# Kernel optimization log

Measured on AMD Instinct MI355X. Metric: run time of the kernel, lower is better.

## Reference

```python
import jax, jax.numpy as jnp
import numpy as np

D = 4          # latent_dims = 2 * 2
POS = 3        # pos_dims = 2 + pos_sorted
HID = 20       # encoder hidden width
LOG_2PI = float(np.log(2.0 * np.pi))


def _fill_scale_tril(vec, d):
    # FillScaleTriL(diag=Exp): lower-tri fill, exp on the diagonal
    idx = jnp.tril_indices(d)
    L = jnp.zeros((d, d), vec.dtype).at[idx].set(vec)
    dg = jnp.diag(L)
    return L - jnp.diag(dg) + jnp.diag(jnp.exp(dg))


def _forward(x, eps, enc_w1, enc_b1, enc_wx, enc_bx, enc_wl, enc_bl,
             dec_w, dec_b, A, b_kf, q_param):
    d = A.shape[0]
    I = jnp.eye(d, dtype=x.dtype)
    # ---- encoder (shared params over time axis, per-object) ----
    h = jax.nn.relu(x @ enc_w1 + enc_b1)            # [T+1, N, HID]
    xhat = h @ enc_wx + enc_bx                       # [T+1, N, d]
    sigma = jnp.exp(0.5 * (h @ enc_wl + enc_bl))     # [T+1, N, d]
    R = sigma[..., :, None] * I                      # diag obs covs [T+1, N, d, d]
    m0, P0 = xhat[0], R[0]                           # initial state per object [N, d]
    zm, zC = xhat[1:], R[1:]                         # measurements [T, N, d], [T, N, d, d]
    # ---- Q = L L^T via CholeskyOuterProduct(FillScaleTriL(q_param)) ----
    L = _fill_scale_tril(q_param, d)
    Q = L @ L.T
    logN = jnp.log(jnp.asarray(zm.shape[1], x.dtype))

    def filter_one(m0_, P0_):
        # PDA Kalman filter for one track over all N measurements per step
        def step(carry, inp):
            m, P = carry
            z, Rz = inp                              # [N, d], [N, d, d]
            mp = A @ m + b_kf
            Pp = A @ P @ A.T + Q
            S = Pp[None] + Rz                        # innovation covs [N, d, d]
            innov = z - mp                           # [N, d]
            sol = jnp.linalg.solve(S, innov[..., None])[..., 0]
            _, logdet = jnp.linalg.slogdet(S)
            ll = -0.5 * (jnp.einsum('nd,nd->n', innov, sol) + logdet + d * LOG_2PI)
            w = jax.nn.softmax(ll)                   # association weights
            # K = Pp S^{-1} (S, Pp symmetric)
            K = jnp.linalg.solve(S, jnp.broadcast_to(Pp, S.shape)).transpose(0, 2, 1)
            mi = mp + jnp.einsum('nij,nj->ni', K, innov)
            Pi = (I - K) @ Pp
            mu = jnp.einsum('n,ni->i', w, mi)
            diff = mi - mu
            Pu = jnp.einsum('n,nij->ij', w, Pi + diff[:, :, None] * diff[:, None, :])
            Pu = 0.5 * (Pu + Pu.T)
            step_ll = jax.nn.logsumexp(ll) - logN    # marginal over associations
            return (mu, Pu), (mu, Pu, mp, Pp, step_ll)

        _, (fm, fP, pm, pP, lls) = jax.lax.scan(step, (m0_, P0_), (zm, zC))

        # ---- RTS smoother (backward pass) ----
        def back(carry, inp):
            ms, Ps = carry
            mf, Pf = inp
            mp = A @ mf + b_kf
            Pp = A @ Pf @ A.T + Q
            G = jnp.linalg.solve(Pp, A @ Pf).T       # Pf A^T Pp^{-1}
            ms2 = mf + G @ (ms - mp)
            Ps2 = Pf + G @ (Ps - Pp) @ G.T
            Ps2 = 0.5 * (Ps2 + Ps2.T)
            return (ms2, Ps2), (ms2, Ps2)

        _, (sm, sP) = jax.lax.scan(back, (fm[-1], fP[-1]), (fm[:-1], fP[:-1]), reverse=True)
        sm = jnp.concatenate([sm, fm[-1:]], 0)
        sP = jnp.concatenate([sP, fP[-1:]], 0)
        return fm, fP, pm, pP, sm, sP, lls

    # vmap over tracks; out_axes=1 puts object axis second ([T, N, ...])
    fm, fP, pm, pP, sm, sP, lls = jax.vmap(filter_one, in_axes=0, out_axes=1)(m0, P0)

    # reparameterized sample from q (smoothed posterior) and decode
    Lc = jnp.linalg.cholesky(sP + 1e-5 * I)          # [T, N, d, d]
    z_recon = sm + jnp.einsum('tnij,tnj->tni', Lc, eps)
    x_recon = z_recon @ dec_w + dec_b                # [T, N, POS]
    return x_recon


def setup_inputs() -> dict:
    key = jax.random.key(0)
    ks = jax.random.split(key, 12)
    Tp1, N = 2049, 64
    s = lambda fan: 1.0 / np.sqrt(fan)
    return {
        'x': jax.random.normal(ks[0], (Tp1, N, POS), jnp.float32),
        'eps': jax.random.normal(ks[1], (Tp1 - 1, N, D), jnp.float32),
        'enc_w1': jax.random.normal(ks[2], (POS, HID), jnp.float32) * s(POS),
        'enc_b1': jnp.zeros((HID,), jnp.float32),
        'enc_wx': jax.random.normal(ks[3], (HID, D), jnp.float32) * s(HID),
        'enc_bx': jnp.zeros((D,), jnp.float32),
        'enc_wl': jax.random.normal(ks[4], (HID, D), jnp.float32) * s(HID),
        'enc_bl': jnp.zeros((D,), jnp.float32),
        'dec_w': jax.random.normal(ks[5], (D, POS), jnp.float32) * s(D),
        'dec_b': jnp.zeros((POS,), jnp.float32),
        'A': jnp.eye(D, dtype=jnp.float32) + 0.01 * jax.random.normal(ks[6], (D, D), jnp.float32),
        'b_kf': jnp.zeros((D,), jnp.float32),
        'q_param': 0.02 * jax.random.normal(ks[7], (D * (D + 1) // 2,), jnp.float32),
    }


def reference(x, eps, enc_w1, enc_b1, enc_wx, enc_bx, enc_wl, enc_bl,
              dec_w, dec_b, A, b_kf, q_param):
    return _forward(x, eps, enc_w1, enc_b1, enc_wx, enc_bx, enc_wl, enc_bl,
                    dec_w, dec_b, A, b_kf, q_param)
```

## Files before the change

### kernel.cpp

```cpp
#include <hip/hip_runtime.h>
#include <math.h>

#define D4   4
#define NB   64
#define T    2048
#define TP1  2049
#define HID  20
#define POS  3
#define CH   64
#define CLEN 32

#define OFF_XHAT  0
#define OFF_SIGMA (TP1*NB*4)
#define OFF_FR    (2*TP1*NB*4)
#define OFF_C     (OFF_FR + T*NB*16)
#define OFF_E     (OFF_C + NB*CH*36)

template<int CTRL, int RM>
__device__ __forceinline__ float dpp_sum_step(float v) {
  int t = __builtin_amdgcn_update_dpp(0, __float_as_int(v), CTRL, RM, 0xF, true);
  return v + __int_as_float(t);
}
__device__ __forceinline__ float wsum_v(float v) {
  v = dpp_sum_step<0x111, 0xF>(v);
  v = dpp_sum_step<0x112, 0xF>(v);
  v = dpp_sum_step<0x114, 0xF>(v);
  v = dpp_sum_step<0x118, 0xF>(v);
  v = dpp_sum_step<0x142, 0xA>(v);
  v = dpp_sum_step<0x143, 0xC>(v);
  return v;
}
__device__ __forceinline__ float rdlane(float v, int l) {
  return __int_as_float(__builtin_amdgcn_readlane(__float_as_int(v), l));
}

__device__ __forceinline__ float inv4(const float a[4][4], float inv[4][4]) {
  float s0 = a[0][0]*a[1][1] - a[1][0]*a[0][1];
  float s1 = a[0][0]*a[1][2] - a[1][0]*a[0][2];
  float s2 = a[0][0]*a[1][3] - a[1][0]*a[0][3];
  float s3 = a[0][1]*a[1][2] - a[1][1]*a[0][2];
  float s4 = a[0][1]*a[1][3] - a[1][1]*a[0][3];
  float s5 = a[0][2]*a[1][3] - a[1][2]*a[0][3];
  float c5 = a[2][2]*a[3][3] - a[3][2]*a[2][3];
  float c4 = a[2][1]*a[3][3] - a[3][1]*a[2][3];
  float c3 = a[2][1]*a[3][2] - a[3][1]*a[2][2];
  float c2 = a[2][0]*a[3][3] - a[3][0]*a[2][3];
  float c1 = a[2][0]*a[3][2] - a[3][0]*a[2][2];
  float c0 = a[2][0]*a[3][1] - a[3][0]*a[2][1];
  float det = s0*c5 - s1*c4 + s2*c3 + s3*c2 - s4*c1 + s5*c0;
  float id = __fdividef(1.0f, det);
  inv[0][0] = ( a[1][1]*c5 - a[1][2]*c4 + a[1][3]*c3) * id;
  inv[0][1] = (-a[0][1]*c5 + a[0][2]*c4 - a[0][3]*c3) * id;
  inv[0][2] = ( a[3][1]*s5 - a[3][2]*s4 + a[3][3]*s3) * id;
  inv[0][3] = (-a[2][1]*s5 + a[2][2]*s4 - a[2][3]*s3) * id;
  inv[1][0] = (-a[1][0]*c5 + a[1][2]*c2 - a[1][3]*c1) * id;
  inv[1][1] = ( a[0][0]*c5 - a[0][2]*c2 + a[0][3]*c1) * id;
  inv[1][2] = (-a[3][0]*s5 + a[3][2]*s2 - a[3][3]*s1) * id;
  inv[1][3] = ( a[2][0]*s5 - a[2][2]*s2 + a[2][3]*s1) * id;
  inv[2][0] = ( a[1][0]*c4 - a[1][1]*c2 + a[1][3]*c0) * id;
  inv[2][1] = (-a[0][0]*c4 + a[0][1]*c2 - a[0][3]*c0) * id;
  inv[2][2] = ( a[3][0]*s4 - a[3][1]*s2 + a[3][3]*s0) * id;
  inv[2][3] = (-a[2][0]*s4 + a[2][1]*s2 - a[2][3]*s0) * id;
  inv[3][0] = (-a[1][0]*c3 + a[1][1]*c1 - a[1][2]*c0) * id;
  inv[3][1] = ( a[0][0]*c3 - a[0][1]*c1 + a[0][2]*c0) * id;
  inv[3][2] = (-a[3][0]*s3 + a[3][1]*s1 - a[3][2]*s0) * id;
  inv[3][3] = ( a[2][0]*s3 - a[2][1]*s1 + a[2][2]*s0) * id;
  return det;
}

__device__ __forceinline__ void build_Q(const float* __restrict__ qp, float Q[4][4]) {
  float L[4][4] = {{0.f,0.f,0.f,0.f},{0.f,0.f,0.f,0.f},{0.f,0.f,0.f,0.f},{0.f,0.f,0.f,0.f}};
  L[0][0] = expf(qp[0]);
  L[1][0] = qp[1]; L[1][1] = expf(qp[2]);
  L[2][0] = qp[3]; L[2][1] = qp[4]; L[2][2] = expf(qp[5]);
  L[3][0] = qp[6]; L[3][1] = qp[7]; L[3][2] = qp[8]; L[3][3] = expf(qp[9]);
#pragma unroll
  for (int r = 0; r < 4; ++r)
#pragma unroll
    for (int c = 0; c < 4; ++c) {
      float v = 0.f;
#pragma unroll
      for (int k = 0; k < 4; ++k) v += L[r][k] * L[c][k];
      Q[r][c] = v;
    }
}

__device__ __forceinline__ void load_A_b_Q(const float* __restrict__ Ag,
                                           const float* __restrict__ bg,
                                           const float* __restrict__ qp,
                                           float A[4][4], float b[4], float Q[4][4]) {
#pragma unroll
  for (int r = 0; r < 4; ++r) {
    b[r] = bg[r];
#pragma unroll
    for (int c = 0; c < 4; ++c) A[r][c] = Ag[r * 4 + c];
  }
  build_Q(qp, Q);
}

__device__ __forceinline__ void load_state_raw(const float* __restrict__ p,
                                               float mf[4], float Pf[4][4]) {
  float4 r0 = *(const float4*)&p[0];
  float4 r1 = *(const float4*)&p[4];
  float4 r2 = *(const float4*)&p[8];
  float4 r3 = *(const float4*)&p[12];
  float rW = __fdividef(1.0f, r0.x);
  mf[0]=r0.y*rW; mf[1]=r0.z*rW; mf[2]=r0.w*rW; mf[3]=r1.x*rW;
  Pf[0][0]=fmaf(r1.y,rW,-mf[0]*mf[0]);
  Pf[0][1]=fmaf(r1.z,rW,-mf[0]*mf[1]); Pf[1][0]=Pf[0][1];
  Pf[0][2]=fmaf(r1.w,rW,-mf[0]*mf[2]); Pf[2][0]=Pf[0][2];
  Pf[0][3]=fmaf(r2.x,rW,-mf[0]*mf[3]); Pf[3][0]=Pf[0][3];
  Pf[1][1]=fmaf(r2.y,rW,-mf[1]*mf[1]);
  Pf[1][2]=fmaf(r2.z,rW,-mf[1]*mf[2]); Pf[2][1]=Pf[1][2];
  Pf[1][3]=fmaf(r2.w,rW,-mf[1]*mf[3]); Pf[3][1]=Pf[1][3];
  Pf[2][2]=fmaf(r3.x,rW,-mf[2]*mf[2]);
  Pf[2][3]=fmaf(r3.y,rW,-mf[2]*mf[3]); Pf[3][2]=Pf[2][3];
  Pf[3][3]=fmaf(r3.z,rW,-mf[3]*mf[3]);
}

__global__ void k_encoder(const float* __restrict__ x,
                          const float* __restrict__ w1, const float* __restrict__ b1,
                          const float* __restrict__ wx, const float* __restrict__ bx,
                          const float* __restrict__ wl, const float* __restrict__ bl,
                          float* __restrict__ xhat, float* __restrict__ sigma) {
  int idx = blockIdx.x * blockDim.x + threadIdx.x;
  if (idx >= TP1 * NB) return;
  float x0 = x[idx*3+0], x1 = x[idx*3+1], x2 = x[idx*3+2];
  float xh[4], lm[4];
#pragma unroll
  for (int k = 0; k < 4; ++k) { xh[k] = bx[k]; lm[k] = bl[k]; }
#pragma unroll
  for (int j = 0; j < HID; ++j) {
    float h = x0*w1[0*HID+j] + x1*w1[1*HID+j] + x2*w1[2*HID+j] + b1[j];
    h = fmaxf(h, 0.0f);
#pragma unroll
    for (int k = 0; k < 4; ++k) { xh[k] += h * wx[j*4+k]; lm[k] += h * wl[j*4+k]; }
  }
  *(float4*)&xhat[(size_t)idx*4]  = make_float4(xh[0], xh[1], xh[2], xh[3]);
  *(float4*)&sigma[(size_t)idx*4] = make_float4(expf(0.5f*lm[0]), expf(0.5f*lm[1]),
                                                expf(0.5f*lm[2]), expf(0.5f*lm[3]));
}

__global__ void __launch_bounds__(256, 1) k_filter(
    const float* __restrict__ xhat, const float* __restrict__ sigma,
    const float* __restrict__ Ag, const float* __restrict__ bg,
    const float* __restrict__ qp,
    float* __restrict__ fr) {
  const int fi  = blockIdx.x;
  const int tid = threadIdx.x;
  const int wv  = tid >> 6;
  const int n   = tid & 63;

  __shared__ __align__(16) float xch[2][16];

  int r, c;
  if (n < 10) {
    r = (n < 4) ? 0 : (n < 7) ? 1 : (n < 9) ? 2 : 3;
    c = (n < 4) ? n : (n < 7) ? n - 3 : (n < 9) ? n - 5 : 3;
  } else if (n < 14) { r = n - 10; c = 0; }
  else { r = 0; c = 0; }

  float ar0 = Ag[r*4+0], ar1 = Ag[r*4+1], ar2 = Ag[r*4+2], ar3 = Ag[r*4+3];
  float ac0 = Ag[c*4+0], ac1 = Ag[c*4+1], ac2 = Ag[c*4+2], ac3 = Ag[c*4+3];
  float qmask = (n < 10) ? 1.0f : 0.0f;
  float pmask = (n >= 10 && n < 14) ? 1.0f : 0.0f;
  float wp0 = (ar0*ac0) * qmask;
  float wp1 = (ar0*ac1 + ar1*ac0) * qmask;
  float wp2 = (ar0*ac2 + ar2*ac0) * qmask;
  float wp3 = (ar0*ac3 + ar3*ac0) * qmask;
  float wp4 = (ar1*ac1) * qmask;
  float wp5 = (ar1*ac2 + ar2*ac1) * qmask;
  float wp6 = (ar1*ac3 + ar3*ac1) * qmask;
  float wp7 = (ar2*ac2) * qmask;
  float wp8 = (ar2*ac3 + ar3*ac2) * qmask;
  float wp9 = (ar3*ac3) * qmask;

  float initv;
  {
    int trir = r*(r+1)/2, tric = c*(c+1)/2;
    float Lr[4], Lc[4];
#pragma unroll
    for (int k = 0; k < 4; ++k) {
      Lr[k] = (k > r) ? 0.0f : (k == r ? expf(qp[trir+r]) : qp[trir+k]);
      Lc[k] = (k > c) ? 0.0f : (k == c ? expf(qp[tric+c]) : qp[tric+k]);
    }
    float Qe = Lr[0]*Lc[0] + Lr[1]*Lc[1] + Lr[2]*Lc[2] + Lr[3]*Lc[3];
    if (n < 10)      initv = Qe;
    else if (n < 14) initv = bg[n-10];
    else             initv = 0.0f;
  }

  float4 A0, A1, A2, A3;
  {
    float4 m0 = *(const float4*)&xhat[fi*4];
    float4 s0 = *(const float4*)&sigma[fi*4];
    A0 = make_float4(1.0f, m0.x, m0.y, m0.z);
    A1 = make_float4(m0.w,
                     fmaf(m0.x, m0.x, s0.x), m0.x*m0.y, m0.x*m0.z);
    A2 = make_float4(m0.x*m0.w,
                     fmaf(m0.y, m0.y, s0.y), m0.y*m0.z, m0.y*m0.w);
    A3 = make_float4(fmaf(m0.z, m0.z, s0.z), m0.z*m0.w,
                     fmaf(m0.w, m0.w, s0.w), 0.0f);
  }

  float4 zz  = *(const float4*)&xhat[(size_t)(NB + n)*4];
  float4 sgc = *(const float4*)&sigma[(size_t)(NB + n)*4];

#pragma unroll 2
  for (int t = 0; t < T; ++t) {
    int nr = (t + 2 <= TP1 - 1) ? (t + 2) : (TP1 - 1);
    float4 zn  = *(const float4*)&xhat[((size_t)nr*NB + n)*4];
    float4 sgn = *(const float4*)&sigma[((size_t)nr*NB + n)*4];

    float rW = __fdividef(1.0f, A0.x);
    float dotq =
        ((fmaf(wp0, A1.y, wp1*A1.z) + fmaf(wp2, A1.w, wp3*A2.x)) +
         (fmaf(wp4, A2.y, wp5*A2.z) + fmaf(wp6, A2.w, wp7*A3.x))) +
        fmaf(wp8, A3.y, wp9*A3.z);
    float wdr = fmaf(ar0, A0.y, ar1*A0.z) + fmaf(ar2, A0.w, ar3*A1.x);
    float wdc = fmaf(ac0, A0.y, ac1*A0.z) + fmaf(ac2, A0.w, ac3*A1.x);
    float Amur = wdr * rW, Amuc = wdc * rW;
    float pe = fmaf(dotq, rW, initv);
    pe = fmaf(pmask, Amur, pe);
    pe = fmaf(-qmask, Amur*Amuc, pe);

    float p00 = rdlane(pe, 0), p01 = rdlane(pe, 1), p02 = rdlane(pe, 2), p03 = rdlane(pe, 3);
    float p11 = rdlane(pe, 4), p12 = rdlane(pe, 5), p13 = rdlane(pe, 6);
    float p22 = rdlane(pe, 7), p23 = rdlane(pe, 8), p33 = rdlane(pe, 9);
    float mp0 = rdlane(pe,10), mp1 = rdlane(pe,11), mp2 = rdlane(pe,12), mp3 = rdlane(pe,13);

    float s00 = p00 + sgc.x, s11 = p11 + sgc.y, s22 = p22 + sgc.z, s33 = p33 + sgc.w;
    float s01 = p01, s02 = p02, s03 = p03, s12 = p12, s13 = p13, s23 = p23;

    float m0_ = s00*s11 - s01*s01;
    float m1_ = s00*s12 - s01*s02;
    float m2_ = s00*s13 - s01*s03;
    float m3_ = s01*s12 - s11*s02;
    float m4_ = s01*s13 - s11*s03;
    float m5_ = s02*s13 - s12*s03;
    float n5_ = s22*s33 - s23*s23;
    float n4_ = s12*s33 - s13*s23;
    float n3_ = s12*s23 - s13*s22;
    float n2_ = s02*s33 - s03*s23;
    float n1_ = s02*s23 - s03*s22;
    float det = (fmaf(m0_, n5_, -(m1_*n4_)) + fmaf(m2_, n3_, m3_*n2_)) +
                fmaf(m5_, m5_, -(m4_*n1_));
    float id  = __fdividef(1.0f, det);
    float rsd = __builtin_amdgcn_rsqf(det);
    float a00_ = ( s11*n5_ - s12*n4_ + s13*n3_);
    float a01_ = (-s01*n5_ + s02*n4_ - s03*n3_);
    float a02_ = ( s13*m5_ - s23*m4_ + s33*m3_);
    float a03_ = (-s12*m5_ + s22*m4_ - s23*m3_);
    float a11_ = ( s00*n5_ - s02*n2_ + s03*n1_);
    float a12_ = (-s03*m5_ + s23*m2_ - s33*m1_);
    float a13_ = ( s02*m5_ - s22*m2_ + s23*m1_);
    float a22_ = ( s03*m4_ - s13*m2_ + s33*m0_);
    float a23_ = (-s02*m4_ + s12*m2_ - s23*m0_);
    float a33_ = ( s02*m3_ - s12*m1_ + s22*m0_);

    float iv0 = zz.x - mp0, iv1 = zz.y - mp1, iv2 = zz.z - mp2, iv3 = zz.w - mp3;
    float ya0 = fmaf(a00_, iv0, a01_*iv1) + fmaf(a02_, iv2, a03_*iv3);
    float ya1 = fmaf(a01_, iv0, a11_*iv1) + fmaf(a12_, iv2, a13_*iv3);
    float ya2 = fmaf(a02_, iv0, a12_*iv1) + fmaf(a22_, iv2, a23_*iv3);
    float ya3 = fmaf(a03_, iv0, a13_*iv1) + fmaf(a23_, iv2, a33_*iv3);
    float quad = (fmaf(iv0, ya0, iv1*ya1) + fmaf(iv2, ya2, iv3*ya3)) * id;

    float wi = __expf(-0.5f * quad) * rsd;

    float y0 = ya0*id, y1 = ya1*id, y2 = ya2*id, y3 = ya3*id;
    float mi0 = fmaf(-sgc.x, y0, zz.x);
    float mi1 = fmaf(-sgc.y, y1, zz.y);
    float mi2 = fmaf(-sgc.z, y2, zz.z);
    float mi3 = fmaf(-sgc.w, y3, zz.w);

    const int par = t & 1;
    float* lb = xch[par];

    if (wv == 0) {
      float cW  = wsum_v(wi);
      float cm0 = wsum_v(wi*mi0);
      float cm1 = wsum_v(wi*mi1);
      float cm2 = wsum_v(wi*mi2);
      float cm3 = wsum_v(wi*mi3);
      if (n == 63) {
        *(float4*)&lb[0] = make_float4(cW, cm0, cm1, cm2);
        lb[4] = cm3;
      }
    } else if (wv == 1) {
      float t0 = sgc.x * id;
      float X00 = fmaf(mi0, mi0, sgc.x) - (t0*sgc.x)*a00_;
      float X01 = fmaf(mi0, mi1, -(t0*sgc.y)*a01_);
      float X02 = fmaf(mi0, mi2, -(t0*sgc.z)*a02_);
      float X03 = fmaf(mi0, mi3, -(t0*sgc.w)*a03_);
      float c00 = wsum_v(wi*X00);
      float c01 = wsum_v(wi*X01);
      float c02 = wsum_v(wi*X02);
      float c03 = wsum_v(wi*X03);
      if (n == 63) { lb[5]=c00; lb[6]=c01; lb[7]=c02; lb[8]=c03; }
    } else if (wv == 2) {
      float t1 = sgc.y * id;
      float X11 = fmaf(mi1, mi1, sgc.y) - (t1*sgc.y)*a11_;
      float X12 = fmaf(mi1, mi2, -(t1*sgc.z)*a12_);
      float X13 = fmaf(mi1, mi3, -(t1*sgc.w)*a13_);
      float c11 = wsum_v(wi*X11);
      float c12 = wsum_v(wi*X12);
      float c13 = wsum_v(wi*X13);
      if (n == 63) { lb[9]=c11; lb[10]=c12; lb[11]=c13; }
    } else {
      float t2 = sgc.z * id;
      float t3 = sgc.w * id;
      float X22 = fmaf(mi2, mi2, sgc.z) - (t2*sgc.z)*a22_;
      float X23 = fmaf(mi2, mi3, -(t2*sgc.w)*a23_);
      float X33 = fmaf(mi3, mi3, sgc.w) - (t3*sgc.w)*a33_;
      float c22 = wsum_v(wi*X22);
      float c23 = wsum_v(wi*X23);
      float c33 = wsum_v(wi*X33);
      if (n == 63) {
        *(float2*)&lb[12] = make_float2(c22, c23);
        lb[14] = c33;
      }
    }

    __syncthreads();

    A0 = *(const float4*)&xch[par][0];
    A1 = *(const float4*)&xch[par][4];
    A2 = *(const float4*)&xch[par][8];
    A3 = *(const float4*)&xch[par][12];

    if (wv == 0 && n == 0) {
      float* fp = &fr[((size_t)t*NB + fi)*16];
      *(float4*)&fp[0]  = A0;
      *(float4*)&fp[4]  = A1;
      *(float4*)&fp[8]  = A2;
      *(float4*)&fp[12] = A3;
    }
    zz = zn; sgc = sgn;
  }
}

struct Map { float G[4][4]; float c[4]; float Dm[4][4]; };

__device__ __forceinline__ void map_identity(Map& M) {
#pragma unroll
  for (int r = 0; r < 4; ++r) {
    M.c[r] = 0.f;
#pragma unroll
    for (int cc = 0; cc < 4; ++cc) { M.G[r][cc] = (r==cc)?1.f:0.f; M.Dm[r][cc] = 0.f; }
  }
}

__device__ __forceinline__ void compose(const Map& F, const Map& Sm, Map& R) {
  float G[4][4], cv[4], V[4][4], Dn[4][4];
#pragma unroll
  for (int r = 0; r < 4; ++r)
#pragma unroll
    for (int c = 0; c < 4; ++c)
      G[r][c] = F.G[r][0]*Sm.G[0][c] + F.G[r][1]*Sm.G[1][c]
              + F.G[r][2]*Sm.G[2][c] + F.G[r][3]*Sm.G[3][c];
#pragma unroll
  for (int r = 0; r < 4; ++r)
    cv[r] = F.c[r] + F.G[r][0]*Sm.c[0] + F.G[r][1]*Sm.c[1]
                   + F.G[r][2]*Sm.c[2] + F.G[r][3]*Sm.c[3];
#pragma unroll
  for (int r = 0; r < 4; ++r)
#pragma unroll
    for (int c = 0; c < 4; ++c)
      V[r][c] = F.G[r][0]*Sm.Dm[0][c] + F.G[r][1]*Sm.Dm[1][c]
              + F.G[r][2]*Sm.Dm[2][c] + F.G[r][3]*Sm.Dm[3][c];
#pragma unroll
  for (int r = 0; r < 4; ++r)
#pragma unroll
    for (int c = r; c < 4; ++c) {
      float v = F.Dm[r][c] + V[r][0]*F.G[c][0] + V[r][1]*F.G[c][1]
                           + V[r][2]*F.G[c][2] + V[r][3]*F.G[c][3];
      Dn[r][c] = v; Dn[c][r] = v;
    }
#pragma unroll
  for (int r = 0; r < 4; ++r) {
    R.c[r] = cv[r];
#pragma unroll
    for (int c = 0; c < 4; ++c) { R.G[r][c] = G[r][c]; R.Dm[r][c] = Dn[r][c]; }
  }
}

__device__ __forceinline__ void make_ft(int t, int i,
    const float* __restrict__ fr,
    const float A[4][4], const float b[4], const float Q[4][4], Map& M) {
  float mf[4], Pf[4][4];
  load_state_raw(&fr[((size_t)t*NB + i)*16], mf, Pf);
  float mp[4];
#pragma unroll
  for (int r = 0; r < 4; ++r)
    mp[r] = b[r] + A[r][0]*mf[0] + A[r][1]*mf[1] + A[r][2]*mf[2] + A[r][3]*mf[3];
  float AP[4][4];
#pragma unroll
  for (int r = 0; r < 4; ++r)
#pragma unroll
    for (int c = 0; c < 4; ++c)
      AP[r][c] = A[r][0]*Pf[0][c] + A[r][1]*Pf[1][c] + A[r][2]*Pf[2][c] + A[r][3]*Pf[3][c];
  float Pp[4][4];
#pragma unroll
  for (int r = 0; r < 4; ++r)
#pragma unroll
    for (int c = r; c < 4; ++c) {
      float v = Q[r][c] + AP[r][0]*A[c][0] + AP[r][1]*A[c][1]
                        + AP[r][2]*A[c][2] + AP[r][3]*A[c][3];
      Pp[r][c] = v; Pp[c][r] = v;
    }
  float Ppi[4][4];
  inv4(Pp, Ppi);
  float W[4][4];
#pragma unroll
  for (int r = 0; r < 4; ++r)
#pragma unroll
    for (int c = 0; c < 4; ++c)
      W[r][c] = Pf[r][0]*A[c][0] + Pf[r][1]*A[c][1] + Pf[r][2]*A[c][2] + Pf[r][3]*A[c][3];
#pragma unroll
  for (int r = 0; r < 4; ++r)
#pragma unroll
    for (int c = 0; c < 4; ++c)
      M.G[r][c] = W[r][0]*Ppi[0][c] + W[r][1]*Ppi[1][c] + W[r][2]*Ppi[2][c] + W[r][3]*Ppi[3][c];
#pragma unroll
  for (int r = 0; r < 4; ++r)
    M.c[r] = mf[r] - (M.G[r][0]*mp[0] + M.G[r][1]*mp[1] + M.G[r][2]*mp[2] + M.G[r][3]*mp[3]);
  float V[4][4];
#pragma unroll
  for (int r = 0; r < 4; ++r)
#pragma unroll
    for (int c = 0; c < 4; ++c)
      V[r][c] = M.G[r][0]*Pp[0][c] + M.G[r][1]*Pp[1][c] + M.G[r][2]*Pp[2][c] + M.G[r][3]*Pp[3][c];
#pragma unroll
  for (int r = 0; r < 4; ++r)
#pragma unroll
    for (int c = r; c < 4; ++c) {
      float v = Pf[r][c] - (V[r][0]*M.G[c][0] + V[r][1]*M.G[c][1]
                          + V[r][2]*M.G[c][2] + V[r][3]*M.G[c][3]);
      M.Dm[r][c] = v; M.Dm[c][r] = v;
    }
}

__device__ __forceinline__ void store_map(float* __restrict__ p, const Map& M) {
  *(float4*)&p[0]  = make_float4(M.G[0][0],M.G[0][1],M.G[0][2],M.G[0][3]);
  *(float4*)&p[4]  = make_float4(M.G[1][0],M.G[1][1],M.G[1][2],M.G[1][3]);
  *(float4*)&p[8]  = make_float4(M.G[2][0],M.G[2][1],M.G[2][2],M.G[2][3]);
  *(float4*)&p[12] = make_float4(M.G[3][0],M.G[3][1],M.G[3][2],M.G[3][3]);
  *(float4*)&p[16] = make_float4(M.c[0],M.c[1],M.c[2],M.c[3]);
  *(float4*)&p[20] = make_float4(M.Dm[0][0],M.Dm[0][1],M.Dm[0][2],M.Dm[0][3]);
  *(float4*)&p[24] = make_float4(M.Dm[1][0],M.Dm[1][1],M.Dm[1][2],M.Dm[1][3]);
  *(float4*)&p[28] = make_float4(M.Dm[2][0],M.Dm[2][1],M.Dm[2][2],M.Dm[2][3]);
  *(float4*)&p[32] = make_float4(M.Dm[3][0],M.Dm[3][1],M.Dm[3][2],M.Dm[3][3]);
}
__device__ __forceinline__ void load_map(const float* __restrict__ p, Map& M) {
  float4 g0=*(const float4*)&p[0], g1=*(const float4*)&p[4],
         g2=*(const float4*)&p[8], g3=*(const float4*)&p[12];
  float4 cv=*(const float4*)&p[16];
  float4 d0=*(const float4*)&p[20], d1=*(const float4*)&p[24],
         d2=*(const float4*)&p[28], d3=*(const float4*)&p[32];
  M.G[0][0]=g0.x;M.G[0][1]=g0.y;M.G[0][2]=g0.z;M.G[0][3]=g0.w;
  M.G[1][0]=g1.x;M.G[1][1]=g1.y;M.G[1][2]=g1.z;M.G[1][3]=g1.w;
  M.G[2][0]=g2.x;M.G[2][1]=g2.y;M.G[2][2]=g2.z;M.G[2][3]=g2.w;
  M.G[3][0]=g3.x;M.G[3][1]=g3.y;M.G[3][2]=g3.z;M.G[3][3]=g3.w;
  M.c[0]=cv.x;M.c[1]=cv.y;M.c[2]=cv.z;M.c[3]=cv.w;
  M.Dm[0][0]=d0.x;M.Dm[0][1]=d0.y;M.Dm[0][2]=d0.z;M.Dm[0][3]=d0.w;
  M.Dm[1][0]=d1.x;M.Dm[1][1]=d1.y;M.Dm[1][2]=d1.z;M.Dm[1][3]=d1.w;
  M.Dm[2][0]=d2.x;M.Dm[2][1]=d2.y;M.Dm[2][2]=d2.z;M.Dm[2][3]=d2.w;
  M.Dm[3][0]=d3.x;M.Dm[3][1]=d3.y;M.Dm[3][2]=d3.z;M.Dm[3][3]=d3.w;
}

__global__ void __launch_bounds__(64, 1) k_phaseA(
    const float* __restrict__ fr,
    const float* __restrict__ Ag, const float* __restrict__ bg,
    const float* __restrict__ qp, float* __restrict__ Cw) {
  const int cc = blockIdx.x;
  const int i  = threadIdx.x;
  float A[4][4], Q[4][4], b[4];
  load_A_b_Q(Ag, bg, qp, A, b, Q);
  Map agg; map_identity(agg);
  int a = cc * CLEN;
  int bb = a + CLEN - 1; if (bb > T - 2) bb = T - 2;
  for (int t = bb; t >= a; --t) {
    Map f; make_ft(t, i, fr, A, b, Q, f);
    compose(f, agg, agg);
  }
  store_map(&Cw[((size_t)i*CH + cc)*36], agg);
}

__global__ void __launch_bounds__(64, 1) k_phaseB(
    const float* __restrict__ Cw, float* __restrict__ Ew) {
  const int i = threadIdx.x;
  Map agg; map_identity(agg);
  for (int cc = CH - 1; cc >= 0; --cc) {
    store_map(&Ew[((size_t)i*CH + cc)*36], agg);
    Map Cc; load_map(&Cw[((size_t)i*CH + cc)*36], Cc);
    compose(Cc, agg, agg);
  }
}

__device__ __forceinline__ void recon(int t, int i,
    const float sm[4], const float sP[4][4],
    const float* __restrict__ eps, const float* __restrict__ dw,
    const float* __restrict__ db, float* __restrict__ out) {
  float a00 = sP[0][0]+1e-5f, a11 = sP[1][1]+1e-5f, a22 = sP[2][2]+1e-5f, a33 = sP[3][3]+1e-5f;
  float L00 = sqrtf(a00);
  float r0 = __fdividef(1.0f, L00);
  float L10 = sP[1][0]*r0, L20 = sP[2][0]*r0, L30 = sP[3][0]*r0;
  float L11 = sqrtf(a11 - L10*L10);
  float r1 = __fdividef(1.0f, L11);
  float L21 = (sP[2][1]-L20*L10)*r1, L31 = (sP[3][1]-L30*L10)*r1;
  float L22 = sqrtf(a22 - L20*L20 - L21*L21);
  float r2 = __fdividef(1.0f, L22);
  float L32 = (sP[3][2]-L30*L20-L31*L21)*r2;
  float L33 = sqrtf(a33 - L30*L30 - L31*L31 - L32*L32);
  float4 e = *(const float4*)&eps[((size_t)t*NB + i)*4];
  float z0 = sm[0] + L00*e.x;
  float z1 = sm[1] + L10*e.x + L11*e.y;
  float z2 = sm[2] + L20*e.x + L21*e.y + L22*e.z;
  float z3 = sm[3] + L30*e.x + L31*e.y + L32*e.z + L33*e.w;
#pragma unroll
  for (int p = 0; p < 3; ++p)
    out[((size_t)t*NB + i)*3 + p] =
        db[p] + z0*dw[0*3+p] + z1*dw[1*3+p] + z2*dw[2*3+p] + z3*dw[3*3+p];
}

__global__ void __launch_bounds__(64, 1) k_phaseC(
    const float* __restrict__ fr,
    const float* __restrict__ Ew,
    const float* __restrict__ Ag, const float* __restrict__ bg,
    const float* __restrict__ qp,
    const float* __restrict__ eps, const float* __restrict__ dw,
    const float* __restrict__ db, float* __restrict__ out) {
  const int cc = blockIdx.x;
  const int i  = threadIdx.x;
  float A[4][4], Q[4][4], b[4];
  load_A_b_Q(Ag, bg, qp, A, b, Q);

  float mT[4], PT[4][4];
  load_state_raw(&fr[((size_t)(T-1)*NB + i)*16], mT, PT);

  Map E; load_map(&Ew[((size_t)i*CH + cc)*36], E);

  float sm[4], sP[4][4];
#pragma unroll
  for (int r = 0; r < 4; ++r)
    sm[r] = E.c[r] + E.G[r][0]*mT[0] + E.G[r][1]*mT[1] + E.G[r][2]*mT[2] + E.G[r][3]*mT[3];
  {
    float V[4][4];
#pragma unroll
    for (int r = 0; r < 4; ++r)
#pragma unroll
      for (int c = 0; c < 4; ++c)
        V[r][c] = E.G[r][0]*PT[0][c] + E.G[r][1]*PT[1][c] + E.G[r][2]*PT[2][c] + E.G[r][3]*PT[3][c];
#pragma unroll
    for (int r = 0; r < 4; ++r)
#pragma unroll
      for (int c = r; c < 4; ++c) {
        float v = E.Dm[r][c] + V[r][0]*E.G[c][0] + V[r][1]*E.G[c][1]
                             + V[r][2]*E.G[c][2] + V[r][3]*E.G[c][3];
        sP[r][c] = v; sP[c][r] = v;
      }
  }

  if (cc == CH - 1) recon(T - 1, i, mT, PT, eps, dw, db, out);

  int a = cc * CLEN;
  int bb = a + CLEN - 1; if (bb > T - 2) bb = T - 2;
  for (int t = bb; t >= a; --t) {
    Map f; make_ft(t, i, fr, A, b, Q, f);
    float smn[4];
#pragma unroll
    for (int r = 0; r < 4; ++r)
      smn[r] = f.c[r] + f.G[r][0]*sm[0] + f.G[r][1]*sm[1] + f.G[r][2]*sm[2] + f.G[r][3]*sm[3];
    float V[4][4];
#pragma unroll
    for (int r = 0; r < 4; ++r)
#pragma unroll
      for (int c = 0; c < 4; ++c)
        V[r][c] = f.G[r][0]*sP[0][c] + f.G[r][1]*sP[1][c] + f.G[r][2]*sP[2][c] + f.G[r][3]*sP[3][c];
#pragma unroll
    for (int r = 0; r < 4; ++r)
#pragma unroll
      for (int c = r; c < 4; ++c) {
        float v = f.Dm[r][c] + V[r][0]*f.G[c][0] + V[r][1]*f.G[c][1]
                             + V[r][2]*f.G[c][2] + V[r][3]*f.G[c][3];
        sP[r][c] = v; sP[c][r] = v;
      }
    sm[0]=smn[0]; sm[1]=smn[1]; sm[2]=smn[2]; sm[3]=smn[3];
    recon(t, i, sm, sP, eps, dw, db, out);
  }
}

extern "C" void kernel_launch(void* const* d_in, const int* in_sizes, int n_in,
                              void* d_out, int out_size, void* d_ws, size_t ws_size,
                              hipStream_t stream) {
  const float* x   = (const float*)d_in[0];
  const float* eps = (const float*)d_in[1];
  const float* w1  = (const float*)d_in[2];
  const float* b1  = (const float*)d_in[3];
  const float* wx  = (const float*)d_in[4];
  const float* bx  = (const float*)d_in[5];
  const float* wl  = (const float*)d_in[6];
  const float* bl  = (const float*)d_in[7];
  const float* dw  = (const float*)d_in[8];
  const float* db  = (const float*)d_in[9];
  const float* Ag  = (const float*)d_in[10];
  const float* bg  = (const float*)d_in[11];
  const float* qp  = (const float*)d_in[12];

  float* ws    = (float*)d_ws;
  float* xhat  = ws + OFF_XHAT;
  float* sigma = ws + OFF_SIGMA;
  float* fr    = ws + OFF_FR;
  float* Cw    = ws + OFF_C;
  float* Ew    = ws + OFF_E;
  float* out   = (float*)d_out;

  k_encoder<<<(TP1*NB + 255)/256, 256, 0, stream>>>(x, w1, b1, wx, bx, wl, bl, xhat, sigma);
  k_filter<<<NB, 256, 0, stream>>>(xhat, sigma, Ag, bg, qp, fr);
  k_phaseA<<<CH, NB, 0, stream>>>(fr, Ag, bg, qp, Cw);
  k_phaseB<<<1, NB, 0, stream>>>(Cw, Ew);
  k_phaseC<<<CH, NB, 0, stream>>>(fr, Ew, Ag, bg, qp, eps, dw, db, out);
}
```

Before: 1.733 ms.

## Parallelize smoother chunk aggregation with LDS Hillis-Steele scan and finer chunks

Replaces the serial per-track backward composition of chunk maps in phase B with a parallel suffix scan in shared memory: one block per track, one thread per chunk, running log2(CH) compose rounds. The chunk count grows from 64 to 256 with chunk length 8, which shortens the serial loops in phases A and C and gives them more blocks. The determinant reciprocal is now taken as the square of the rsq result instead of a separate divide. The scan does more total compose work and adds barriers. The rsq-squared reciprocal is only valid for a positive determinant and may lose some precision.

```diff
diff --git a/kernel.cpp b/kernel.cpp
--- a/kernel.cpp
+++ b/kernel.cpp
@@ -7,8 +7,8 @@
 #define TP1  2049
 #define HID  20
 #define POS  3
-#define CH   64
-#define CLEN 32
+#define CH   256
+#define CLEN 8
 
 #define OFF_XHAT  0
 #define OFF_SIGMA (TP1*NB*4)
@@ -245,8 +245,8 @@
     float n1_ = s02*s23 - s03*s22;
     float det = (fmaf(m0_, n5_, -(m1_*n4_)) + fmaf(m2_, n3_, m3_*n2_)) +
                 fmaf(m5_, m5_, -(m4_*n1_));
-    float id  = __fdividef(1.0f, det);
     float rsd = __builtin_amdgcn_rsqf(det);
+    float id  = rsd * rsd;
     float a00_ = ( s11*n5_ - s12*n4_ + s13*n3_);
     float a01_ = (-s01*n5_ + s02*n4_ - s03*n3_);
     float a02_ = ( s13*m5_ - s23*m4_ + s33*m3_);
@@ -468,6 +468,29 @@
   M.Dm[3][0]=d3.x;M.Dm[3][1]=d3.y;M.Dm[3][2]=d3.z;M.Dm[3][3]=d3.w;
 }
 
+__device__ __forceinline__ void store_map_lds(float* p, const Map& M) {
+#pragma unroll
+  for (int r = 0; r < 4; ++r) {
+#pragma unroll
+    for (int c2 = 0; c2 < 4; ++c2) {
+      p[r*4+c2]    = M.G[r][c2];
+      p[20+r*4+c2] = M.Dm[r][c2];
+    }
+    p[16+r] = M.c[r];
+  }
+}
+__device__ __forceinline__ void load_map_lds(const float* p, Map& M) {
+#pragma unroll
+  for (int r = 0; r < 4; ++r) {
+#pragma unroll
+    for (int c2 = 0; c2 < 4; ++c2) {
+      M.G[r][c2]  = p[r*4+c2];
+      M.Dm[r][c2] = p[20+r*4+c2];
+    }
+    M.c[r] = p[16+r];
+  }
+}
+
 __global__ void __launch_bounds__(64, 1) k_phaseA(
     const float* __restrict__ fr,
     const float* __restrict__ Ag, const float* __restrict__ bg,
@@ -486,15 +509,35 @@
   store_map(&Cw[((size_t)i*CH + cc)*36], agg);
 }
 
-__global__ void __launch_bounds__(64, 1) k_phaseB(
+__global__ void __launch_bounds__(CH, 1) k_phaseB(
     const float* __restrict__ Cw, float* __restrict__ Ew) {
-  const int i = threadIdx.x;
-  Map agg; map_identity(agg);
-  for (int cc = CH - 1; cc >= 0; --cc) {
-    store_map(&Ew[((size_t)i*CH + cc)*36], agg);
-    Map Cc; load_map(&Cw[((size_t)i*CH + cc)*36], Cc);
-    compose(Cc, agg, agg);
-  }
+  const int fi = blockIdx.x;
+  const int cc = threadIdx.x;
+  __shared__ float lds[CH * 37];
+
+  Map M;
+  load_map(&Cw[((size_t)fi*CH + cc)*36], M);
+  store_map_lds(&lds[cc*37], M);
+  __syncthreads();
+
+#pragma unroll
+  for (int k = 0; k < 8; ++k) {
+    int step = 1 << k;
+    Map P;
+    bool have = (cc + step < CH);
+    if (have) load_map_lds(&lds[(cc+step)*37], P);
+    __syncthreads();
+    if (have) {
+      compose(M, P, M);
+      store_map_lds(&lds[cc*37], M);
+    }
+    __syncthreads();
+  }
+
+  Map E;
+  if (cc == CH - 1) map_identity(E);
+  else              load_map_lds(&lds[(cc+1)*37], E);
+  store_map(&Ew[((size_t)fi*CH + cc)*36], E);
 }
 
 __device__ __forceinline__ void recon(int t, int i,
@@ -618,6 +661,6 @@
   k_encoder<<<(TP1*NB + 255)/256, 256, 0, stream>>>(x, w1, b1, wx, bx, wl, bl, xhat, sigma);
   k_filter<<<NB, 256, 0, stream>>>(xhat, sigma, Ag, bg, qp, fr);
   k_phaseA<<<CH, NB, 0, stream>>>(fr, Ag, bg, qp, Cw);
-  k_phaseB<<<1, NB, 0, stream>>>(Cw, Ew);
+  k_phaseB<<<NB, CH, 0, stream>>>(Cw, Ew);
   k_phaseC<<<CH, NB, 0, stream>>>(fr, Ew, Ag, bg, qp, eps, dw, db, out);
 }
```

After: 1.578 ms (median of 2 runs). 1.1x faster.
